# Performance work log

Hardware: AMD Instinct MI355X
Metric: run time of the kernel (lower is better)

## Reference

```python
import jax, jax.numpy as jnp
import numpy as np

D = 64  # neighbor_co_occurrence_feat_dim
B, S = 256, 512
VOCAB = 100

def setup_inputs() -> dict:
    key = jax.random.key(0)
    k1, k2, k3, k4, k5, k6 = jax.random.split(key, 6)
    src_neighbor_ids = jax.random.randint(k1, (B, S), 0, VOCAB, dtype=jnp.int64)
    dst_neighbor_ids = jax.random.randint(k2, (B, S), 0, VOCAB, dtype=jnp.int64)
    # Linear(2, D) then Linear(D, D); store weights as [in, out] for direct matmul
    W1 = jax.random.normal(k3, (2, D), dtype=jnp.float32) * (1.0 / np.sqrt(2.0))
    b1 = jax.random.normal(k4, (D,), dtype=jnp.float32) * 0.01
    W2 = jax.random.normal(k5, (D, D), dtype=jnp.float32) * (1.0 / np.sqrt(D))
    b2 = jax.random.normal(k6, (D,), dtype=jnp.float32) * 0.01
    return {"src_neighbor_ids": src_neighbor_ids, "dst_neighbor_ids": dst_neighbor_ids,
            "W1": W1, "b1": b1, "W2": W2, "b2": b2}

def _count_in(query, keys):
    # query: [B,S] ids; keys: [B,S] ids -> [B,S] count of query[i,j] within keys[i,:]
    return jnp.sum(query[:, :, None] == keys[:, None, :], axis=2).astype(jnp.float32)

def _appearances(ids, src_ids, dst_ids):
    c_src = _count_in(ids, src_ids)  # [B,S]
    c_dst = _count_in(ids, dst_ids)  # [B,S]
    feats = jnp.stack([c_src, c_dst], axis=-1)  # [B,S,2]
    mask = (ids != 0).astype(jnp.float32)[:, :, None]  # padding id 0 -> zero features
    return feats * mask

def _encode(x, W1, b1, W2, b2):
    h = jax.nn.relu(x @ W1 + b1)
    return h @ W2 + b2

def reference(src_neighbor_ids, dst_neighbor_ids, W1, b1, W2, b2):
    src_app = _appearances(src_neighbor_ids, src_neighbor_ids, dst_neighbor_ids)
    dst_app = _appearances(dst_neighbor_ids, src_neighbor_ids, dst_neighbor_ids)
    src_features = _encode(src_app, W1, b1, W2, b2)
    dst_features = _encode(dst_app, W1, b1, W2, b2)
    return (src_features, dst_features)
```

## Files before the change

kernel.cpp:

```cpp
#include <hip/hip_runtime.h>

#define BATCH 256
#define SEQ   512
#define DIM   64
#define VOC   100
#define NTHREADS 512
#define ENC_PITCH 68

__global__ __launch_bounds__(NTHREADS)
void ncoe_kernel(const int* __restrict__ src_ids,
                 const int* __restrict__ dst_ids,
                 const float* __restrict__ W1,
                 const float* __restrict__ b1,
                 const float* __restrict__ W2,
                 const float* __restrict__ b2,
                 float* __restrict__ out)
{
    __shared__ __align__(16) float sW2[DIM][DIM];
    __shared__ __align__(16) float sW1[2][DIM];
    __shared__ __align__(16) float sb1[DIM];
    __shared__ __align__(16) float sb2[DIM];
    __shared__ __align__(16) float enc[VOC][ENC_PITCH];
    __shared__ int hist_s[104];
    __shared__ int hist_d[104];

    const int t   = threadIdx.x;
    const int row = blockIdx.x;

    if (t < 104) { hist_s[t] = 0; hist_d[t] = 0; }
    {
        const float4* W2v  = (const float4*)W2;
        float4*       sW2v = (float4*)&sW2[0][0];
        sW2v[t]       = W2v[t];
        sW2v[t + 512] = W2v[t + 512];
        if (t < 32)      ((float4*)&sW1[0][0])[t] = ((const float4*)W1)[t];
        else if (t < 48) ((float4*)sb1)[t - 32]   = ((const float4*)b1)[t - 32];
        else if (t < 64) ((float4*)sb2)[t - 48]   = ((const float4*)b2)[t - 48];
    }
    __syncthreads();

    {
        int a = src_ids[row * SEQ + t];
        int b = dst_ids[row * SEQ + t];
        atomicAdd(&hist_s[a], 1);
        atomicAdd(&hist_d[b], 1);
    }
    __syncthreads();

    if (t < 400) {
        const int tv = t >> 4;
        const int to = t & 15;
        const int vbase = tv * 4;
        const int obase = to * 4;

        float av[4], bv[4];
        #pragma unroll
        for (int r = 0; r < 4; ++r) {
            int v = vbase + r;
            av[r] = (v == 0) ? 0.f : (float)hist_s[v];
            bv[r] = (v == 0) ? 0.f : (float)hist_d[v];
        }

        float acc[4][4];
        #pragma unroll
        for (int r = 0; r < 4; ++r)
            #pragma unroll
            for (int c = 0; c < 4; ++c)
                acc[r][c] = sb2[obase + c];

        #pragma unroll 8
        for (int d = 0; d < DIM; ++d) {
            float w10 = sW1[0][d];
            float w11 = sW1[1][d];
            float bb  = sb1[d];
            float4 w2 = *(const float4*)&sW2[d][obase];
            #pragma unroll
            for (int r = 0; r < 4; ++r) {
                float h = fmaxf(0.f, fmaf(av[r], w10, fmaf(bv[r], w11, bb)));
                acc[r][0] = fmaf(h, w2.x, acc[r][0]);
                acc[r][1] = fmaf(h, w2.y, acc[r][1]);
                acc[r][2] = fmaf(h, w2.z, acc[r][2]);
                acc[r][3] = fmaf(h, w2.w, acc[r][3]);
            }
        }

        #pragma unroll
        for (int r = 0; r < 4; ++r) {
            float4 res = make_float4(acc[r][0], acc[r][1], acc[r][2], acc[r][3]);
            *(float4*)&enc[vbase + r][obase] = res;
        }
    }
    __syncthreads();

    float4* out4 = (float4*)out;
    const size_t rowOff = (size_t)row * (SEQ * DIM / 4);
    const size_t dstOff = (size_t)BATCH * (size_t)(SEQ * DIM / 4);
    #pragma unroll
    for (int k = 0; k < (SEQ * DIM / 4) / NTHREADS; ++k) {
        int it = t + k * NTHREADS;
        int j  = it >> 4;
        int q  = (it & 15) << 2;
        int vs = src_ids[row * SEQ + j];
        int vd = dst_ids[row * SEQ + j];
        float4 r1 = *(const float4*)&enc[vs][q];
        float4 r2 = *(const float4*)&enc[vd][q];
        out4[rowOff + it]          = r1;
        out4[dstOff + rowOff + it] = r2;
    }
}

extern "C" void kernel_launch(void* const* d_in, const int* in_sizes, int n_in,
                              void* d_out, int out_size, void* d_ws, size_t ws_size,
                              hipStream_t stream) {
    const int*   src = (const int*)d_in[0];
    const int*   dst = (const int*)d_in[1];
    const float* W1  = (const float*)d_in[2];
    const float* b1  = (const float*)d_in[3];
    const float* W2  = (const float*)d_in[4];
    const float* b2  = (const float*)d_in[5];
    ncoe_kernel<<<BATCH, NTHREADS, 0, stream>>>(src, dst, W1, b1, W2, b2, (float*)d_out);
}
```

Before: 25.15 us.

## Split into per-row encode kernel and grid-wide gather kernel via workspace

Splits the fused per-row kernel into two launches. The first builds the per-row vocabulary encoding table and writes it to a global workspace. The second is a gather kernel with 2048 blocks that spreads the output writes across many more blocks than the original 256. This aims to raise occupancy and memory parallelism for the write-dominated gather, at the cost of an extra launch and a round trip of the encoding table through global memory (about 6.5MB). It falls back to the fused kernel when the workspace is too small.

Measured after the change: 36.03 us. 43.3% more time.

```diff
diff --git a/kernel.cpp b/kernel.cpp
--- a/kernel.cpp
+++ b/kernel.cpp
@@ -7,14 +7,125 @@
 #define NTHREADS 512
 #define ENC_PITCH 68
 
+#define K2_BLOCKS  2048
+#define K2_THREADS 256
+
 __global__ __launch_bounds__(NTHREADS)
-void ncoe_kernel(const int* __restrict__ src_ids,
-                 const int* __restrict__ dst_ids,
-                 const float* __restrict__ W1,
-                 const float* __restrict__ b1,
-                 const float* __restrict__ W2,
-                 const float* __restrict__ b2,
-                 float* __restrict__ out)
+void enc_kernel(const int* __restrict__ src_ids,
+                const int* __restrict__ dst_ids,
+                const float* __restrict__ W1,
+                const float* __restrict__ b1,
+                const float* __restrict__ W2,
+                const float* __restrict__ b2,
+                float4* __restrict__ enc_ws)
+{
+    __shared__ __align__(16) float sW2[DIM][DIM];
+    __shared__ __align__(16) float sW1[2][DIM];
+    __shared__ __align__(16) float sb1[DIM];
+    __shared__ __align__(16) float sb2[DIM];
+    __shared__ int hist_s[104];
+    __shared__ int hist_d[104];
+
+    const int t   = threadIdx.x;
+    const int row = blockIdx.x;
+
+    if (t < 104) { hist_s[t] = 0; hist_d[t] = 0; }
+    {
+        const float4* W2v  = (const float4*)W2;
+        float4*       sW2v = (float4*)&sW2[0][0];
+        sW2v[t]       = W2v[t];
+        sW2v[t + 512] = W2v[t + 512];
+        if (t < 32)      ((float4*)&sW1[0][0])[t] = ((const float4*)W1)[t];
+        else if (t < 48) ((float4*)sb1)[t - 32]   = ((const float4*)b1)[t - 32];
+        else if (t < 64) ((float4*)sb2)[t - 48]   = ((const float4*)b2)[t - 48];
+    }
+    __syncthreads();
+
+    {
+        int a = src_ids[row * SEQ + t];
+        int b = dst_ids[row * SEQ + t];
+        atomicAdd(&hist_s[a], 1);
+        atomicAdd(&hist_d[b], 1);
+    }
+    __syncthreads();
+
+    if (t < 400) {
+        const int tv = t >> 4;
+        const int to = t & 15;
+        const int vbase = tv * 4;
+        const int obase = to * 4;
+
+        float av[4], bv[4];
+        #pragma unroll
+        for (int r = 0; r < 4; ++r) {
+            int v = vbase + r;
+            av[r] = (v == 0) ? 0.f : (float)hist_s[v];
+            bv[r] = (v == 0) ? 0.f : (float)hist_d[v];
+        }
+
+        float acc[4][4];
+        #pragma unroll
+        for (int r = 0; r < 4; ++r)
+            #pragma unroll
+            for (int c = 0; c < 4; ++c)
+                acc[r][c] = sb2[obase + c];
+
+        #pragma unroll 8
+        for (int d = 0; d < DIM; ++d) {
+            float w10 = sW1[0][d];
+            float w11 = sW1[1][d];
+            float bb  = sb1[d];
+            float4 w2 = *(const float4*)&sW2[d][obase];
+            #pragma unroll
+            for (int r = 0; r < 4; ++r) {
+                float h = fmaxf(0.f, fmaf(av[r], w10, fmaf(bv[r], w11, bb)));
+                acc[r][0] = fmaf(h, w2.x, acc[r][0]);
+                acc[r][1] = fmaf(h, w2.y, acc[r][1]);
+                acc[r][2] = fmaf(h, w2.z, acc[r][2]);
+                acc[r][3] = fmaf(h, w2.w, acc[r][3]);
+            }
+        }
+
+        #pragma unroll
+        for (int r = 0; r < 4; ++r) {
+            float4 res = make_float4(acc[r][0], acc[r][1], acc[r][2], acc[r][3]);
+            enc_ws[((size_t)(row * VOC + vbase + r) << 4) + to] = res;
+        }
+    }
+}
+
+__global__ __launch_bounds__(K2_THREADS)
+void gather_kernel(const int* __restrict__ src_ids,
+                   const int* __restrict__ dst_ids,
+                   const float4* __restrict__ enc_ws,
+                   float4* __restrict__ out4)
+{
+    const int tot = BATCH * SEQ * (DIM / 4);
+    int u = blockIdx.x * K2_THREADS + threadIdx.x;
+    const int stride = K2_BLOCKS * K2_THREADS;
+    #pragma unroll
+    for (int k = 0; k < 4; ++k, u += stride) {
+        int row = u >> 13;
+        int j   = (u >> 4) & (SEQ - 1);
+        int q   = u & 15;
+        int idx = row * SEQ + j;
+        int vs  = src_ids[idx];
+        int vd  = dst_ids[idx];
+        float4 r1 = enc_ws[((size_t)(row * VOC + vs) << 4) | q];
+        float4 r2 = enc_ws[((size_t)(row * VOC + vd) << 4) | q];
+        out4[u]       = r1;
+        out4[tot + u] = r2;
+    }
+}
+
+__global__ __launch_bounds__(NTHREADS)
+void ncoe_fused_kernel(const int* __restrict__ src_ids,
+                       const int* __restrict__ dst_ids,
+                       const float* __restrict__ W1,
+                       const float* __restrict__ b1,
+                       const float* __restrict__ W2,
+                       const float* __restrict__ b2,
+                       float* __restrict__ out)
 {
     __shared__ __align__(16) float sW2[DIM][DIM];
     __shared__ __align__(16) float sW1[2][DIM];
@@ -118,5 +229,13 @@
     const float* b1  = (const float*)d_in[3];
     const float* W2  = (const float*)d_in[4];
     const float* b2  = (const float*)d_in[5];
-    ncoe_kernel<<<BATCH, NTHREADS, 0, stream>>>(src, dst, W1, b1, W2, b2, (float*)d_out);
-}
+
+    const size_t enc_bytes = (size_t)BATCH * VOC * DIM * sizeof(float);
+    if (ws_size >= enc_bytes) {
+        float4* enc_ws = (float4*)d_ws;
+        enc_kernel<<<BATCH, NTHREADS, 0, stream>>>(src, dst, W1, b1, W2, b2, enc_ws);
+        gather_kernel<<<K2_BLOCKS, K2_THREADS, 0, stream>>>(src, dst, enc_ws, (float4*)d_out);
+    } else {
+        ncoe_fused_kernel<<<BATCH, NTHREADS, 0, stream>>>(src, dst, W1, b1, W2, b2, (float*)d_out);
+    }
+}
```

## Split each row across two blocks by output half, cache ids, use nontemporal stores

Applied to the files above, without the earlier changes.

Launches two blocks per batch row, each computing and writing only half of the 64 output features. This doubles the grid to 512 blocks for better occupancy on the many CUs. Neighbor ids are staged once in shared memory and reused in the output phase instead of being reloaded from global memory. Output writes use nontemporal stores to avoid cache pollution. In exchange, the histogram and id loads are duplicated across the two half-blocks.

Result: faster. 22.73 us (-9.6%).

```diff
diff --git a/kernel.cpp b/kernel.cpp
--- a/kernel.cpp
+++ b/kernel.cpp
@@ -3,9 +3,12 @@
 #define BATCH 256
 #define SEQ   512
 #define DIM   64
+#define HALF  32
 #define VOC   100
 #define NTHREADS 512
-#define ENC_PITCH 68
+#define ENC_PITCH 36
+
+typedef float f32x4 __attribute__((ext_vector_type(4)));
 
 __global__ __launch_bounds__(NTHREADS)
 void ncoe_kernel(const int* __restrict__ src_ids,
@@ -14,42 +17,42 @@
                  const float* __restrict__ b1,
                  const float* __restrict__ W2,
                  const float* __restrict__ b2,
-                 float* __restrict__ out)
+                 f32x4* __restrict__ out4)
 {
-    __shared__ __align__(16) float sW2[DIM][DIM];
+    __shared__ __align__(16) float sW2h[DIM][HALF];
     __shared__ __align__(16) float sW1[2][DIM];
     __shared__ __align__(16) float sb1[DIM];
-    __shared__ __align__(16) float sb2[DIM];
+    __shared__ __align__(16) float sb2h[HALF];
     __shared__ __align__(16) float enc[VOC][ENC_PITCH];
+    __shared__ int sSrc[SEQ];
+    __shared__ int sDst[SEQ];
     __shared__ int hist_s[104];
     __shared__ int hist_d[104];
 
-    const int t   = threadIdx.x;
-    const int row = blockIdx.x;
+    const int t    = threadIdx.x;
+    const int row  = blockIdx.x >> 1;
+    const int half = blockIdx.x & 1;
 
     if (t < 104) { hist_s[t] = 0; hist_d[t] = 0; }
     {
-        const float4* W2v  = (const float4*)W2;
-        float4*       sW2v = (float4*)&sW2[0][0];
-        sW2v[t]       = W2v[t];
-        sW2v[t + 512] = W2v[t + 512];
-        if (t < 32)      ((float4*)&sW1[0][0])[t] = ((const float4*)W1)[t];
-        else if (t < 48) ((float4*)sb1)[t - 32]   = ((const float4*)b1)[t - 32];
-        else if (t < 64) ((float4*)sb2)[t - 48]   = ((const float4*)b2)[t - 48];
+        const int d = t >> 3, c = t & 7;
+        ((f32x4*)&sW2h[0][0])[t] =
+            ((const f32x4*)W2)[d * (DIM / 4) + half * (HALF / 4) + c];
+        if (t < 32)      ((f32x4*)&sW1[0][0])[t] = ((const f32x4*)W1)[t];
+        else if (t < 48) ((f32x4*)sb1)[t - 32]   = ((const f32x4*)b1)[t - 32];
+        else if (t < 56) ((f32x4*)sb2h)[t - 48]  = ((const f32x4*)b2)[half * (HALF / 4) + t - 48];
+        sSrc[t] = src_ids[row * SEQ + t];
+        sDst[t] = dst_ids[row * SEQ + t];
     }
     __syncthreads();
 
-    {
-        int a = src_ids[row * SEQ + t];
-        int b = dst_ids[row * SEQ + t];
-        atomicAdd(&hist_s[a], 1);
-        atomicAdd(&hist_d[b], 1);
-    }
+    atomicAdd(&hist_s[sSrc[t]], 1);
+    atomicAdd(&hist_d[sDst[t]], 1);
     __syncthreads();
 
-    if (t < 400) {
-        const int tv = t >> 4;
-        const int to = t & 15;
+    if (t < 200) {
+        const int tv = t >> 3;
+        const int to = t & 7;
         const int vbase = tv * 4;
         const int obase = to * 4;
 
@@ -66,14 +69,14 @@
         for (int r = 0; r < 4; ++r)
             #pragma unroll
             for (int c = 0; c < 4; ++c)
-                acc[r][c] = sb2[obase + c];
+                acc[r][c] = sb2h[obase + c];
 
         #pragma unroll 8
         for (int d = 0; d < DIM; ++d) {
             float w10 = sW1[0][d];
             float w11 = sW1[1][d];
             float bb  = sb1[d];
-            float4 w2 = *(const float4*)&sW2[d][obase];
+            f32x4 w2 = *(const f32x4*)&sW2h[d][obase];
             #pragma unroll
             for (int r = 0; r < 4; ++r) {
                 float h = fmaxf(0.f, fmaf(av[r], w10, fmaf(bv[r], w11, bb)));
@@ -86,26 +89,25 @@
 
         #pragma unroll
         for (int r = 0; r < 4; ++r) {
-            float4 res = make_float4(acc[r][0], acc[r][1], acc[r][2], acc[r][3]);
-            *(float4*)&enc[vbase + r][obase] = res;
+            f32x4 res = { acc[r][0], acc[r][1], acc[r][2], acc[r][3] };
+            *(f32x4*)&enc[vbase + r][obase] = res;
         }
     }
     __syncthreads();
 
-    float4* out4 = (float4*)out;
-    const size_t rowOff = (size_t)row * (SEQ * DIM / 4);
-    const size_t dstOff = (size_t)BATCH * (size_t)(SEQ * DIM / 4);
+    const int tot = BATCH * SEQ * (DIM / 4);
     #pragma unroll
-    for (int k = 0; k < (SEQ * DIM / 4) / NTHREADS; ++k) {
+    for (int k = 0; k < (SEQ * (HALF / 4)) / NTHREADS; ++k) {
         int it = t + k * NTHREADS;
-        int j  = it >> 4;
-        int q  = (it & 15) << 2;
-        int vs = src_ids[row * SEQ + j];
-        int vd = dst_ids[row * SEQ + j];
-        float4 r1 = *(const float4*)&enc[vs][q];
-        float4 r2 = *(const float4*)&enc[vd][q];
-        out4[rowOff + it]          = r1;
-        out4[dstOff + rowOff + it] = r2;
+        int j  = it >> 3;
+        int q  = it & 7;
+        int vs = sSrc[j];
+        int vd = sDst[j];
+        f32x4 r1 = *(const f32x4*)&enc[vs][q * 4];
+        f32x4 r2 = *(const f32x4*)&enc[vd][q * 4];
+        size_t o = (((size_t)(row * SEQ + j)) << 4) + half * (HALF / 4) + q;
+        __builtin_nontemporal_store(r1, &out4[o]);
+        __builtin_nontemporal_store(r2, &out4[tot + o]);
     }
 }
 
@@ -118,5 +120,5 @@
     const float* b1  = (const float*)d_in[3];
     const float* W2  = (const float*)d_in[4];
     const float* b2  = (const float*)d_in[5];
-    ncoe_kernel<<<BATCH, NTHREADS, 0, stream>>>(src, dst, W1, b1, W2, b2, (float*)d_out);
+    ncoe_kernel<<<BATCH * 2, NTHREADS, 0, stream>>>(src, dst, W1, b1, W2, b2, (f32x4*)d_out);
 }
```
